# Kernel optimization log

Measured on AMD Instinct MI355X. Metric: run time of the kernel, lower is better.

Reference implementation:

```python
import jax, jax.numpy as jnp
import numpy as np


def setup_inputs() -> dict:
    key = jax.random.key(0)
    ks = jax.random.split(key, 32)
    def rn(i, shape, s=0.02):
        return jax.random.normal(ks[i], shape, dtype=jnp.float32) * s
    z = lambda n: jnp.zeros((n,), dtype=jnp.float32)
    return {
        'c2': rn(0, (8, 256, 112, 112), 1.0),
        'c3': rn(1, (8, 512, 56, 56), 1.0),
        'c4': rn(2, (8, 1024, 28, 28), 1.0),
        'c5': rn(3, (8, 2048, 14, 14), 1.0),
        'lat_w0': rn(4, (256, 256)),  'lat_b0': z(256),
        'lat_w1': rn(5, (512, 256)),  'lat_b1': z(256),
        'lat_w2': rn(6, (1024, 256)), 'lat_b2': z(256),
        'lat_w3': rn(7, (2048, 256)), 'lat_b3': z(256),
        'sp_w1': rn(8, (2048, 512)), 'sp_b1': z(512),
        'sp_w2': rn(9, (512, 4)),    'sp_b2': z(4),
        'qkv_w': rn(10, (256, 768)), 'qkv_b': z(768),
        'proj_w': rn(11, (256, 256)), 'proj_b': z(256),
        'gat_W': rn(12, (4, 256, 256)),
        'gat_a': rn(13, (4, 512)),
        'out_w': rn(14, (1024, 256)), 'out_b': z(256),
        'label_emb': rn(15, (80, 256), 1.0),
        'spec_w1': rn(16, (256, 128)), 'spec_b1': z(128),
        'spec_w2': rn(17, (128, 80)),  'spec_b2': z(80),
        'spat_w1': rn(18, (256, 128)), 'spat_b1': z(128),
        'spat_w2': rn(19, (128, 80)),  'spat_b2': z(80),
        'gate_w': rn(20, (256, 80)), 'gate_b': z(80),
        'unc_w': rn(21, (256, 80)),  'unc_b': z(80),
    }


def _forward(c2, c3, c4, c5,
             lat_w0, lat_b0, lat_w1, lat_b1, lat_w2, lat_b2, lat_w3, lat_b3,
             sp_w1, sp_b1, sp_w2, sp_b2,
             qkv_w, qkv_b, proj_w, proj_b,
             gat_W, gat_a, out_w, out_b, label_emb,
             spec_w1, spec_b1, spec_w2, spec_b2,
             spat_w1, spat_b1, spat_w2, spat_b2,
             gate_w, gate_b, unc_w, unc_b):
    B = c2.shape[0]
    L = label_emb.shape[0]
    C = 256
    # --- DynamicScaleAwareFPN ---
    pooled = c5.mean(axis=(2, 3))                                   # [B,2048]
    sw = jax.nn.softmax(jax.nn.relu(pooled @ sp_w1 + sp_b1) @ sp_w2 + sp_b2, axis=1)  # [B,4]
    H, W = c2.shape[2], c2.shape[3]
    feats = (c2, c3, c4, c5)
    lws = (lat_w0, lat_w1, lat_w2, lat_w3)
    lbs = (lat_b0, lat_b1, lat_b2, lat_b3)
    fused = jnp.zeros((B, C, H, W), dtype=c2.dtype)
    for i in range(4):  # fixed 4 scales
        l = jnp.einsum('bchw,cd->bdhw', feats[i], lws[i]) + lbs[i][None, :, None, None]
        if l.shape[2] != H or l.shape[3] != W:
            l = jax.image.resize(l, (B, C, H, W), method='bilinear')  # align_corners=False
        fused = fused + l * sw[:, i, None, None, None]
    # --- DeformableAttention (N=H*W > max_tokens=196 -> adaptive pool to 14x14) ---
    th = 14
    x = fused.reshape(B, C, th, H // th, th, W // th).mean(axis=(3, 5))  # exact adaptive avg pool
    x = x.reshape(B, C, th * th).transpose(0, 2, 1)                      # [B,196,C]
    N, nh, hd = th * th, 8, C // 8
    qkv = (x @ qkv_w + qkv_b).reshape(B, N, 3, nh, hd).transpose(2, 0, 3, 1, 4)
    q, k, v = qkv[0], qkv[1], qkv[2]                                     # [B,nh,N,hd]
    attn = jax.nn.softmax(jnp.einsum('bhnd,bhmd->bhnm', q, k) * (hd ** -0.5), axis=-1)
    xo = jnp.einsum('bhnm,bhmd->bhnd', attn, v).transpose(0, 2, 1, 3).reshape(B, N, C)
    xo = xo @ proj_w + proj_b
    gctx = xo.mean(axis=1)                                               # [B,C]
    # --- CrossLabelSemanticGraph (4 GAT heads) ---
    lf = label_emb[None] + gctx[:, None, :]                              # [B,L,C]
    def gat(Wm, avec):
        Wx = lf @ Wm                                                     # [B,L,C]
        # a([Wx_i ; Wx_j]) = Wx_i @ a1 + Wx_j @ a2  (avoids O(L^2*2C) tensor)
        s1 = Wx @ avec[:C]                                               # [B,L]
        s2 = Wx @ avec[C:]                                               # [B,L]
        e = jax.nn.leaky_relu(s1[:, :, None] + s2[:, None, :], 0.2)      # [B,L,L]
        att = jax.nn.softmax(e, axis=2)
        return att @ Wx, att
    heads, atts = jax.vmap(gat)(gat_W, gat_a)                            # [4,B,L,C],[4,B,L,L]
    concat = jnp.moveaxis(heads, 0, 2).reshape(B, L, 4 * C)              # head-order concat
    graph = concat @ out_w + out_b                                       # [B,L,C]
    agg = graph.mean(axis=1)                                             # [B,C]
    # --- SpectralSpatialFusion (dropout inactive at eval) ---
    spec = jax.nn.relu(agg @ spec_w1 + spec_b1) @ spec_w2 + spec_b2
    spat = jax.nn.relu(agg @ spat_w1 + spat_b1) @ spat_w2 + spat_b2
    gate = jax.nn.sigmoid(agg @ gate_w + gate_b)
    logits = gate * spec + (1.0 - gate) * spat
    # --- UncertaintyHead ---
    alpha = jax.nn.softplus(agg @ unc_w + unc_b) + 1.0
    unc = L / jnp.sum(alpha, axis=1, keepdims=True)
    return (logits, spec, spat, gate, unc, sw, atts)


def reference(c2, c3, c4, c5,
              lat_w0, lat_b0, lat_w1, lat_b1, lat_w2, lat_b2, lat_w3, lat_b3,
              sp_w1, sp_b1, sp_w2, sp_b2,
              qkv_w, qkv_b, proj_w, proj_b,
              gat_W, gat_a, out_w, out_b, label_emb,
              spec_w1, spec_b1, spec_w2, spec_b2,
              spat_w1, spat_b1, spat_w2, spat_b2,
              gate_w, gate_b, unc_w, unc_b):
    return _forward(c2, c3, c4, c5,
                    lat_w0, lat_b0, lat_w1, lat_b1, lat_w2, lat_b2, lat_w3, lat_b3,
                    sp_w1, sp_b1, sp_w2, sp_b2,
                    qkv_w, qkv_b, proj_w, proj_b,
                    gat_W, gat_a, out_w, out_b, label_emb,
                    spec_w1, spec_b1, spec_w2, spec_b2,
                    spat_w1, spat_b1, spat_w2, spat_b2,
                    gate_w, gate_b, unc_w, unc_b)
```

## Files before the change

kernel.cpp:

```cpp
#include <hip/hip_runtime.h>
#include <math.h>

typedef __attribute__((ext_vector_type(8))) short bshort8;
typedef __attribute__((ext_vector_type(4))) float f32x4;

#define DI __device__ __forceinline__

DI unsigned short f2bf(float x) {
    unsigned int u = __builtin_bit_cast(unsigned int, x);
    u += 0x7fffu + ((u >> 16) & 1u);
    return (unsigned short)(u >> 16);
}

DI bshort8 pack8(const float* v) {
    bshort8 r;
    #pragma unroll
    for (int j = 0; j < 8; j++) r[j] = (short)f2bf(v[j]);
    return r;
}

DI f32x4 mfma16(bshort8 a, bshort8 b, f32x4 c) {
    return __builtin_amdgcn_mfma_f32_16x16x32_bf16(a, b, c, 0, 0, 0);
}

__device__ const float W14[14][3] = {
    {0.875f, 0.125f, 0.f},
    {0.125f, 0.75f, 0.125f}, {0.125f, 0.75f, 0.125f}, {0.125f, 0.75f, 0.125f},
    {0.125f, 0.75f, 0.125f}, {0.125f, 0.75f, 0.125f}, {0.125f, 0.75f, 0.125f},
    {0.125f, 0.75f, 0.125f}, {0.125f, 0.75f, 0.125f}, {0.125f, 0.75f, 0.125f},
    {0.125f, 0.75f, 0.125f}, {0.125f, 0.75f, 0.125f}, {0.125f, 0.75f, 0.125f},
    {0.125f, 0.875f, 0.f}};
__device__ const float W28[14][4] = {
    {0.5f, 0.4375f, 0.0625f, 0.f},
    {0.0625f, 0.4375f, 0.4375f, 0.0625f}, {0.0625f, 0.4375f, 0.4375f, 0.0625f},
    {0.0625f, 0.4375f, 0.4375f, 0.0625f}, {0.0625f, 0.4375f, 0.4375f, 0.0625f},
    {0.0625f, 0.4375f, 0.4375f, 0.0625f}, {0.0625f, 0.4375f, 0.4375f, 0.0625f},
    {0.0625f, 0.4375f, 0.4375f, 0.0625f}, {0.0625f, 0.4375f, 0.4375f, 0.0625f},
    {0.0625f, 0.4375f, 0.4375f, 0.0625f}, {0.0625f, 0.4375f, 0.4375f, 0.0625f},
    {0.0625f, 0.4375f, 0.4375f, 0.0625f}, {0.0625f, 0.4375f, 0.4375f, 0.0625f},
    {0.0625f, 0.4375f, 0.5f, 0.f}};
__device__ const float W56[14][6] = {
    {0.25f, 0.25f, 0.25f, 0.21875f, 0.03125f, 0.f},
    {0.03125f, 0.21875f, 0.25f, 0.25f, 0.21875f, 0.03125f},
    {0.03125f, 0.21875f, 0.25f, 0.25f, 0.21875f, 0.03125f},
    {0.03125f, 0.21875f, 0.25f, 0.25f, 0.21875f, 0.03125f},
    {0.03125f, 0.21875f, 0.25f, 0.25f, 0.21875f, 0.03125f},
    {0.03125f, 0.21875f, 0.25f, 0.25f, 0.21875f, 0.03125f},
    {0.03125f, 0.21875f, 0.25f, 0.25f, 0.21875f, 0.03125f},
    {0.03125f, 0.21875f, 0.25f, 0.25f, 0.21875f, 0.03125f},
    {0.03125f, 0.21875f, 0.25f, 0.25f, 0.21875f, 0.03125f},
    {0.03125f, 0.21875f, 0.25f, 0.25f, 0.21875f, 0.03125f},
    {0.03125f, 0.21875f, 0.25f, 0.25f, 0.21875f, 0.03125f},
    {0.03125f, 0.21875f, 0.25f, 0.25f, 0.21875f, 0.03125f},
    {0.03125f, 0.21875f, 0.25f, 0.25f, 0.21875f, 0.03125f},
    {0.03125f, 0.21875f, 0.25f, 0.25f, 0.25f, 0.f}};

template <int N, int C, int TAPS>
__global__ __launch_bounds__(256) void pool_elem(
    const float* __restrict__ src, float* __restrict__ dst)
{
    unsigned id = blockIdx.x * 256u + threadIdx.x;
    unsigned p = id / 196u;
    unsigned r = id - p * 196u;
    unsigned ti = r / 14u, tj = r - ti * 14u;
    unsigned b = p / C, cin = p - b * C;
    const float* plane = src + (size_t)p * (N * N);
    float acc = 0.f;
    if constexpr (N == 112) {
        const float4* p4 = (const float4*)(plane + (size_t)(ti * 8) * 112 + tj * 8);
        #pragma unroll
        for (int i = 0; i < 8; i++) {
            float4 u = p4[i * 28];
            float4 v = p4[i * 28 + 1];
            acc += (u.x + u.y) + (u.z + u.w) + (v.x + v.y) + (v.z + v.w);
        }
        acc *= (1.f / 64.f);
    } else {
        constexpr int STRIDE = N / 14;
        const float (*WT)[TAPS] = (N == 14) ? (const float (*)[TAPS])W14
                                : (N == 28) ? (const float (*)[TAPS])W28
                                            : (const float (*)[TAPS])W56;
        int hs = (int)(STRIDE * ti) - 1; if (hs < 0) hs = 0;
        int ws = (int)(STRIDE * tj) - 1; if (ws < 0) ws = 0;
        float wh[TAPS], ww[TAPS];
        #pragma unroll
        for (int i = 0; i < TAPS; i++) { wh[i] = WT[ti][i]; ww[i] = WT[tj][i]; }
        #pragma unroll
        for (int i = 0; i < TAPS; i++) {
            int hi = hs + i; if (hi > N - 1) hi = N - 1;
            const float* row = plane + (size_t)hi * N;
            float rs = 0.f;
            #pragma unroll
            for (int j = 0; j < TAPS; j++) {
                int wj = ws + j; if (wj > N - 1) wj = N - 1;
                rs += ww[j] * row[wj];
            }
            acc += wh[i] * rs;
        }
    }
    dst[(size_t)cin * 1568 + b * 196 + r] = acc;
}

__global__ __launch_bounds__(256) void c5_mean(
    const float* __restrict__ c5, float* __restrict__ pooled)
{
    int wid = threadIdx.x >> 6, lane = threadIdx.x & 63;
    int p = blockIdx.x * 4 + wid;
    const float* plane = c5 + (size_t)p * 196;
    float v = plane[lane] + plane[64 + lane] + plane[128 + lane];
    if (lane < 4) v += plane[192 + lane];
    #pragma unroll
    for (int off = 32; off > 0; off >>= 1) v += __shfl_xor(v, off, 64);
    if (lane == 0) pooled[p] = v * (1.f / 196.f);
}

__global__ __launch_bounds__(512) void sw_part(
    const float* __restrict__ pooled, const float* __restrict__ sp_w1,
    float* __restrict__ partial)
{
    int b = blockIdx.x, kc = blockIdx.y, t = threadIdx.x;
    __shared__ float ps[256];
    if (t < 256) ps[t] = pooled[b * 2048 + kc * 256 + t];
    __syncthreads();
    float acc = 0.f;
    const float* w = sp_w1 + (size_t)(kc * 256) * 512 + t;
    #pragma unroll 4
    for (int c = 0; c < 256; c++) acc += ps[c] * w[(size_t)c * 512];
    partial[((size_t)b * 8 + kc) * 512 + t] = acc;
}

__global__ __launch_bounds__(512) void sw_fin(
    const float* __restrict__ partial, const float* __restrict__ sp_b1,
    const float* __restrict__ sp_w2, const float* __restrict__ sp_b2,
    const float* __restrict__ lb0, const float* __restrict__ lb1,
    const float* __restrict__ lb2, const float* __restrict__ lb3,
    float* __restrict__ sw_out, float* __restrict__ beff)
{
    int b = blockIdx.x, t = threadIdx.x;
    __shared__ float h[512];
    __shared__ float s4s[4];
    __shared__ float swl[4];
    float a = sp_b1[t];
    #pragma unroll
    for (int kc = 0; kc < 8; kc++) a += partial[((size_t)b * 8 + kc) * 512 + t];
    h[t] = fmaxf(a, 0.f);
    __syncthreads();
    int wv = t >> 6, lane = t & 63;
    if (wv < 4) {
        float acc = 0.f;
        #pragma unroll
        for (int i = 0; i < 8; i++) {
            int idx = lane + 64 * i;
            acc += h[idx] * sp_w2[idx * 4 + wv];
        }
        #pragma unroll
        for (int off = 32; off > 0; off >>= 1) acc += __shfl_xor(acc, off, 64);
        if (lane == 0) s4s[wv] = acc + sp_b2[wv];
    }
    __syncthreads();
    if (t == 0) {
        float mx = fmaxf(fmaxf(s4s[0], s4s[1]), fmaxf(s4s[2], s4s[3]));
        float e0 = expf(s4s[0] - mx), e1 = expf(s4s[1] - mx);
        float e2 = expf(s4s[2] - mx), e3 = expf(s4s[3] - mx);
        float inv = 1.f / (e0 + e1 + e2 + e3);
        swl[0] = e0 * inv; swl[1] = e1 * inv; swl[2] = e2 * inv; swl[3] = e3 * inv;
        for (int o = 0; o < 4; o++) sw_out[b * 4 + o] = swl[o];
    }
    __syncthreads();
    if (t < 256)
        beff[b * 256 + t] = swl[0] * lb0[t] + swl[1] * lb1[t] + swl[2] * lb2[t] + swl[3] * lb3[t];
}

__global__ __launch_bounds__(256) void xtok_init(
    const float* __restrict__ beff, float* __restrict__ xtok)
{
    int m = blockIdx.x, c = threadIdx.x;
    xtok[(size_t)m * 256 + c] = beff[(m / 196) * 256 + c];
}

__global__ __launch_bounds__(256) void lateral_slice(
    const float* __restrict__ pf0, const float* __restrict__ pf1,
    const float* __restrict__ pf2, const float* __restrict__ pf3,
    const float* __restrict__ w0, const float* __restrict__ w1,
    const float* __restrict__ w2, const float* __restrict__ w3,
    const float* __restrict__ sw, float* __restrict__ xtok)
{
    const int sArr[8]    = {0, 1, 2, 2, 3, 3, 3, 3};
    const int koffArr[8] = {0, 0, 0, 512, 0, 512, 1024, 1536};
    const int klenArr[8] = {256, 512, 512, 512, 512, 512, 512, 512};
    int sl = blockIdx.y;
    int s = sArr[sl], koff = koffArr[sl], klen = klenArr[sl];
    const float* pf = (s == 0) ? pf0 : (s == 1) ? pf1 : (s == 2) ? pf2 : pf3;
    const float* W  = (s == 0) ? w0  : (s == 1) ? w1  : (s == 2) ? w2  : w3;

    int mt = blockIdx.x % 49, nt = blockIdx.x / 49;
    int m0 = mt * 32, n0 = nt * 64;
    __shared__ alignas(16) unsigned short As[1024];
    __shared__ alignas(16) unsigned short Bs[2048];
    int t = threadIdx.x, lane = t & 63, wid = t >> 6;
    int wm = wid >> 1, wn = wid & 1;
    f32x4 acc0 = {0, 0, 0, 0}, acc1 = {0, 0, 0, 0};

    int f = t & 63;
    int mA = m0 + ((t >> 6) & 1) * 16 + (f & 15);
    int kbA = (f >> 4) * 8;
    int nB = n0 + (t >> 6) * 16 + (f & 15);
    int kbB = (f >> 4) * 8;
    float swv = sw[(mA / 196) * 4 + s];

    float ar[8], br[8];
    auto loadA = [&](int k0) {
        if (t < 128) {
            const float* base = pf + (size_t)(koff + k0 + kbA) * 1568 + mA;
            #pragma unroll
            for (int j = 0; j < 8; j++) ar[j] = base[(size_t)j * 1568] * swv;
        }
    };
    auto loadB = [&](int k0) {
        const float* base = W + (size_t)(koff + k0 + kbB) * 256 + nB;
        #pragma unroll
        for (int j = 0; j < 8; j++) br[j] = base[(size_t)j * 256];
    };

    loadA(0); loadB(0);
    for (int k0 = 0; k0 < klen; k0 += 32) {
        if (t < 128) *(bshort8*)&As[(((t >> 6) & 1) * 512 + f * 8)] = pack8(ar);
        *(bshort8*)&Bs[((t >> 6) * 512 + f * 8)] = pack8(br);
        __syncthreads();
        if (k0 + 32 < klen) { loadA(k0 + 32); loadB(k0 + 32); }
        bshort8 av = *(const bshort8*)&As[wm * 512 + lane * 8];
        bshort8 bv0 = *(const bshort8*)&Bs[(wn * 2 + 0) * 512 + lane * 8];
        bshort8 bv1 = *(const bshort8*)&Bs[(wn * 2 + 1) * 512 + lane * 8];
        acc0 = mfma16(av, bv0, acc0);
        acc1 = mfma16(av, bv1, acc1);
        __syncthreads();
    }
    int col0 = n0 + wn * 32 + (lane & 15);
    int rbase = m0 + wm * 16 + ((lane >> 4) << 2);
    #pragma unroll
    for (int r = 0; r < 4; r++) {
        int m = rbase + r;
        atomicAdd(&xtok[(size_t)m * 256 + col0], acc0[r]);
        atomicAdd(&xtok[(size_t)m * 256 + col0 + 16], acc1[r]);
    }
}

template <bool B_IS_KXN>
__global__ __launch_bounds__(256) void gemm_kernel(
    const float* __restrict__ Ab, int lda, long long sAy, long long sAz,
    const float* __restrict__ Bb, int ldb, long long sBy, long long sBz,
    float* __restrict__ Cb, int ldc, long long sCy, long long sCz,
    const float* __restrict__ bias, int M, int N, int K,
    float alpha, int mtiles)
{
    const float* A = Ab + blockIdx.y * sAy + blockIdx.z * sAz;
    const float* B = Bb + blockIdx.y * sBy + blockIdx.z * sBz;
    float* C = Cb + blockIdx.y * sCy + blockIdx.z * sCz;
    int mt = blockIdx.x % mtiles, nt = blockIdx.x / mtiles;
    int m0 = mt * 32, n0 = nt * 64;
    __shared__ alignas(16) unsigned short As[1024];
    __shared__ alignas(16) unsigned short Bs[2048];
    int t = threadIdx.x, lane = t & 63, wid = t >> 6;
    int wm = wid >> 1, wn = wid & 1;
    f32x4 acc0 = {0, 0, 0, 0}, acc1 = {0, 0, 0, 0};

    int f = t & 63;
    int mA = m0 + ((t >> 6) & 1) * 16 + (f & 15);
    int kbA = (f >> 4) * 8;
    int nB = n0 + (t >> 6) * 16 + (f & 15);
    int kbB = (f >> 4) * 8;

    float ar[8], br[8];
    auto loadA = [&](int k0) {
        if (t < 128) {
            int kb = k0 + kbA;
            if (mA < M && kb + 8 <= K) {
                const float4* p = (const float4*)(A + (size_t)mA * lda + kb);
                float4 u = p[0], v = p[1];
                ar[0] = u.x; ar[1] = u.y; ar[2] = u.z; ar[3] = u.w;
                ar[4] = v.x; ar[5] = v.y; ar[6] = v.z; ar[7] = v.w;
            } else {
                #pragma unroll
                for (int j = 0; j < 8; j++) {
                    int k = kb + j;
                    ar[j] = (mA < M && k < K) ? A[(size_t)mA * lda + k] : 0.f;
                }
            }
        }
    };
    auto loadB = [&](int k0) {
        int kb = k0 + kbB;
        if constexpr (B_IS_KXN) {
            #pragma unroll
            for (int j = 0; j < 8; j++) {
                int k = kb + j;
                br[j] = (k < K && nB < N) ? B[(size_t)k * ldb + nB] : 0.f;
            }
        } else {
            if (nB < N && kb + 8 <= K) {
                const float4* p = (const float4*)(B + (size_t)nB * ldb + kb);
                float4 u = p[0], v = p[1];
                br[0] = u.x; br[1] = u.y; br[2] = u.z; br[3] = u.w;
                br[4] = v.x; br[5] = v.y; br[6] = v.z; br[7] = v.w;
            } else {
                #pragma unroll
                for (int j = 0; j < 8; j++) {
                    int k = kb + j;
                    br[j] = (nB < N && k < K) ? B[(size_t)nB * ldb + k] : 0.f;
                }
            }
        }
    };

    loadA(0); loadB(0);
    for (int k0 = 0; k0 < K; k0 += 32) {
        if (t < 128) *(bshort8*)&As[(((t >> 6) & 1) * 512 + f * 8)] = pack8(ar);
        *(bshort8*)&Bs[((t >> 6) * 512 + f * 8)] = pack8(br);
        __syncthreads();
        if (k0 + 32 < K) { loadA(k0 + 32); loadB(k0 + 32); }
        bshort8 av = *(const bshort8*)&As[wm * 512 + lane * 8];
        bshort8 bv0 = *(const bshort8*)&Bs[(wn * 2 + 0) * 512 + lane * 8];
        bshort8 bv1 = *(const bshort8*)&Bs[(wn * 2 + 1) * 512 + lane * 8];
        acc0 = mfma16(av, bv0, acc0);
        acc1 = mfma16(av, bv1, acc1);
        __syncthreads();
    }
    int col0 = n0 + wn * 32 + (lane & 15);
    int rbase = m0 + wm * 16 + ((lane >> 4) << 2);
    #pragma unroll
    for (int r = 0; r < 4; r++) {
        int m = rbase + r;
        if (m < M) {
            if (col0 < N) {
                float v = acc0[r] * alpha;
                if (bias) v += bias[col0];
                C[(size_t)m * ldc + col0] = v;
            }
            int c1 = col0 + 16;
            if (c1 < N) {
                float v = acc1[r] * alpha;
                if (bias) v += bias[c1];
                C[(size_t)m * ldc + c1] = v;
            }
        }
    }
}

__global__ __launch_bounds__(256) void attn_softmax(float* __restrict__ S)
{
    int wid = threadIdx.x >> 6, lane = threadIdx.x & 63;
    size_t row = (size_t)blockIdx.x * 4 + wid;
    float* p = S + row * 196;
    float v0 = p[lane];
    float v1 = p[64 + lane];
    float v2 = p[128 + lane];
    float v3 = (lane < 4) ? p[192 + lane] : -1e30f;
    float mx = fmaxf(fmaxf(v0, v1), fmaxf(v2, v3));
    #pragma unroll
    for (int off = 32; off > 0; off >>= 1) mx = fmaxf(mx, __shfl_xor(mx, off, 64));
    float e0 = expf(v0 - mx), e1 = expf(v1 - mx), e2 = expf(v2 - mx);
    float e3 = (lane < 4) ? expf(v3 - mx) : 0.f;
    float sum = e0 + e1 + e2 + e3;
    #pragma unroll
    for (int off = 32; off > 0; off >>= 1) sum += __shfl_xor(sum, off, 64);
    float inv = 1.f / sum;
    p[lane] = e0 * inv;
    p[64 + lane] = e1 * inv;
    p[128 + lane] = e2 * inv;
    if (lane < 4) p[192 + lane] = e3 * inv;
}

__global__ __launch_bounds__(256) void xo_part(
    const float* __restrict__ xo, float* __restrict__ xopart)
{
    int b = blockIdx.x, g = blockIdx.y, t = threadIdx.x;
    const float* base = xo + ((size_t)b * 196 + g * 28) * 256 + t;
    float s = 0.f;
    #pragma unroll
    for (int n = 0; n < 28; n++) s += base[(size_t)n * 256];
    xopart[(b * 7 + g) * 256 + t] = s;
}

__global__ __launch_bounds__(256) void gctx_part(
    const float* __restrict__ xopart, const float* __restrict__ proj_w,
    float* __restrict__ gpart)
{
    int b = blockIdx.x, kc = blockIdx.y, t = threadIdx.x;
    __shared__ float xm[64];
    if (t < 64) {
        float s = 0.f;
        #pragma unroll
        for (int g = 0; g < 7; g++) s += xopart[(b * 7 + g) * 256 + kc * 64 + t];
        xm[t] = s * (1.f / 196.f);
    }
    __syncthreads();
    float acc = 0.f;
    const float* w = proj_w + (size_t)(kc * 64) * 256 + t;
    #pragma unroll 8
    for (int j = 0; j < 64; j++) acc += xm[j] * w[(size_t)j * 256];
    gpart[(b * 4 + kc) * 256 + t] = acc;
}

__global__ __launch_bounds__(256) void lf_write(
    const float* __restrict__ gpart, const float* __restrict__ proj_b,
    const float* __restrict__ lemb, float* __restrict__ lf)
{
    int b = blockIdx.x, l = blockIdx.y, t = threadIdx.x;
    float g = proj_b[t] + gpart[(b * 4 + 0) * 256 + t] + gpart[(b * 4 + 1) * 256 + t]
            + gpart[(b * 4 + 2) * 256 + t] + gpart[(b * 4 + 3) * 256 + t];
    lf[((size_t)b * 80 + l) * 256 + t] = lemb[l * 256 + t] + g;
}

__global__ __launch_bounds__(256) void wa2(
    const float* __restrict__ gat_W, const float* __restrict__ gat_a,
    float* __restrict__ Wa)
{
    int h = blockIdx.x, q = blockIdx.y;
    int t = threadIdx.x, w = t >> 6, lane = t & 63;
    __shared__ float a1[256], a2[256];
    a1[t] = gat_a[h * 512 + t];
    a2[t] = gat_a[h * 512 + 256 + t];
    __syncthreads();
    for (int ci = 0; ci < 16; ci++) {
        int c = q * 64 + w * 16 + ci;
        const float* row = gat_W + (size_t)h * 65536 + (size_t)c * 256;
        float p1 = 0.f, p2 = 0.f;
        #pragma unroll
        for (int jj = 0; jj < 4; jj++) {
            float v = row[lane + 64 * jj];
            p1 += v * a1[lane + 64 * jj];
            p2 += v * a2[lane + 64 * jj];
        }
        #pragma unroll
        for (int off = 32; off > 0; off >>= 1) {
            p1 += __shfl_xor(p1, off, 64);
            p2 += __shfl_xor(p2, off, 64);
        }
        if (lane == 0) { Wa[h * 512 + c] = p1; Wa[h * 512 + 256 + c] = p2; }
    }
}

__global__ __launch_bounds__(256) void s12_kernel(
    const float* __restrict__ lf, const float* __restrict__ Wa,
    float* __restrict__ s12)
{
    int l = blockIdx.x, b = blockIdx.y, t = threadIdx.x, w = t >> 6, lane = t & 63;
    __shared__ float row[256];
    row[t] = lf[((size_t)b * 80 + l) * 256 + t];
    __syncthreads();
    #pragma unroll
    for (int pp = 0; pp < 2; pp++) {
        int pair = w * 2 + pp;
        float p = 0.f;
        #pragma unroll
        for (int jj = 0; jj < 4; jj++) {
            int c = lane + 64 * jj;
            p += row[c] * Wa[pair * 256 + c];
        }
        #pragma unroll
        for (int off = 32; off > 0; off >>= 1) p += __shfl_xor(p, off, 64);
        if (lane == 0) s12[(b * 8 + pair) * 80 + l] = p;
    }
}

__global__ __launch_bounds__(256) void gat_rows(
    const float* __restrict__ s12, float* __restrict__ atts)
{
    int b = blockIdx.x, h = blockIdx.y, z = blockIdx.z;
    int t = threadIdx.x, w = t >> 6, lane = t & 63;
    int i = z * 4 + w;
    float s1i = s12[(b * 8 + h * 2) * 80 + i];
    const float* s2 = s12 + (b * 8 + h * 2 + 1) * 80;
    float v0 = s1i + s2[lane]; v0 = v0 > 0.f ? v0 : 0.2f * v0;
    float v1 = -1e30f;
    if (lane < 16) { v1 = s1i + s2[64 + lane]; v1 = v1 > 0.f ? v1 : 0.2f * v1; }
    float mx = fmaxf(v0, v1);
    #pragma unroll
    for (int off = 32; off > 0; off >>= 1) mx = fmaxf(mx, __shfl_xor(mx, off, 64));
    float e0 = expf(v0 - mx), e1 = (lane < 16) ? expf(v1 - mx) : 0.f;
    float sum = e0 + e1;
    #pragma unroll
    for (int off = 32; off > 0; off >>= 1) sum += __shfl_xor(sum, off, 64);
    float inv = 1.f / sum;
    float* orow = atts + (size_t)h * 51200 + b * 6400 + i * 80;
    orow[lane] = e0 * inv;
    if (lane < 16) orow[64 + lane] = e1 * inv;
}

__global__ __launch_bounds__(256) void amlf_kernel(
    const float* __restrict__ atts, const float* __restrict__ lf,
    float* __restrict__ amlf)
{
    int b = blockIdx.x, h = blockIdx.y, t = threadIdx.x;
    __shared__ float am[80];
    if (t < 80) {
        const float* base = atts + (size_t)h * 51200 + b * 6400 + t;
        float acc = 0.f;
        for (int l = 0; l < 80; l++) acc += base[l * 80];
        am[t] = acc * (1.f / 80.f);
    }
    __syncthreads();
    float acc = 0.f;
    const float* lfb = lf + (size_t)b * 80 * 256 + t;
    #pragma unroll 4
    for (int l = 0; l < 80; l++) acc += am[l] * lfb[(size_t)l * 256];
    amlf[(b * 4 + h) * 256 + t] = acc;
}

__global__ __launch_bounds__(256) void hm_part(
    const float* __restrict__ amlf, const float* __restrict__ gat_W,
    float* __restrict__ hmpart)
{
    int b = blockIdx.x, h = blockIdx.y, kc = blockIdx.z, t = threadIdx.x;
    __shared__ float av[64];
    if (t < 64) av[t] = amlf[(b * 4 + h) * 256 + kc * 64 + t];
    __syncthreads();
    float acc = 0.f;
    const float* w = gat_W + (size_t)h * 65536 + (size_t)(kc * 64) * 256 + t;
    #pragma unroll 8
    for (int j = 0; j < 64; j++) acc += av[j] * w[(size_t)j * 256];
    hmpart[((b * 4 + h) * 4 + kc) * 256 + t] = acc;
}

__global__ __launch_bounds__(256) void as_part(
    const float* __restrict__ hmpart, const float* __restrict__ out_w,
    float* __restrict__ aspart)
{
    int b = blockIdx.x, kc = blockIdx.y, t = threadIdx.x;
    __shared__ float hv[64];
    if (t < 64) {
        int hk = kc * 64 + t;
        int h = hk >> 8, c = hk & 255;
        const float* p = hmpart + ((size_t)(b * 4 + h) * 4) * 256 + c;
        hv[t] = p[0] + p[256] + p[512] + p[768];
    }
    __syncthreads();
    float acc = 0.f;
    const float* w = out_w + (size_t)(kc * 64) * 256 + t;
    #pragma unroll 8
    for (int j = 0; j < 64; j++) acc += hv[j] * w[(size_t)j * 256];
    aspart[(b * 16 + kc) * 256 + t] = acc;
}

__global__ __launch_bounds__(256) void final2(
    const float* __restrict__ aspart, const float* __restrict__ out_b,
    const float* __restrict__ spec_w1, const float* __restrict__ spec_b1,
    const float* __restrict__ spec_w2, const float* __restrict__ spec_b2,
    const float* __restrict__ spat_w1, const float* __restrict__ spat_b1,
    const float* __restrict__ spat_w2, const float* __restrict__ spat_b2,
    const float* __restrict__ gate_w, const float* __restrict__ gate_b,
    const float* __restrict__ unc_w, const float* __restrict__ unc_b,
    float* __restrict__ out)
{
    int b = blockIdx.x, t = threadIdx.x;
    __shared__ float a_s[256], h1[128], h2[128];
    __shared__ float spv[80], stv[80], gzv[80], alph[80];
    float acc = out_b[t];
    #pragma unroll
    for (int kc = 0; kc < 16; kc++) acc += aspart[(b * 16 + kc) * 256 + t];
    a_s[t] = acc;
    __syncthreads();
    {
        int o = t & 127;
        const float* w1 = (t < 128) ? spec_w1 : spat_w1;
        float a1 = (t < 128) ? spec_b1[o] : spat_b1[o];
        #pragma unroll 4
        for (int c = 0; c < 256; c++) a1 += a_s[c] * w1[c * 128 + o];
        if (t < 128) h1[o] = fmaxf(a1, 0.f); else h2[o] = fmaxf(a1, 0.f);
    }
    __syncthreads();
    if (t < 80) {
        float sp = spec_b2[t];
        for (int c = 0; c < 128; c++) sp += h1[c] * spec_w2[c * 80 + t];
        float gz = gate_b[t];
        #pragma unroll 4
        for (int c = 0; c < 256; c++) gz += a_s[c] * gate_w[c * 80 + t];
        spv[t] = sp; gzv[t] = gz;
    } else if (t >= 128 && t < 208) {
        int o = t - 128;
        float st = spat_b2[o];
        for (int c = 0; c < 128; c++) st += h2[c] * spat_w2[c * 80 + o];
        float uz = unc_b[o];
        #pragma unroll 4
        for (int c = 0; c < 256; c++) uz += a_s[c] * unc_w[c * 80 + o];
        stv[o] = st; alph[o] = log1pf(expf(uz)) + 1.f;
    }
    __syncthreads();
    if (t < 80) {
        float g = 1.f / (1.f + expf(-gzv[t]));
        out[b * 80 + t] = g * spv[t] + (1.f - g) * stv[t];
        out[640 + b * 80 + t] = spv[t];
        out[1280 + b * 80 + t] = stv[t];
        out[1920 + b * 80 + t] = g;
    }
    __syncthreads();
    if (t == 0) {
        float s = 0.f;
        for (int l = 0; l < 80; l++) s += alph[l];
        out[2560 + b] = 80.f / s;
    }
}

extern "C" void kernel_launch(void* const* d_in, const int* in_sizes, int n_in,
                              void* d_out, int out_size, void* d_ws, size_t ws_size,
                              hipStream_t stream)
{
    (void)in_sizes; (void)n_in; (void)out_size; (void)ws_size;
    const float* c2 = (const float*)d_in[0];
    const float* c3 = (const float*)d_in[1];
    const float* c4 = (const float*)d_in[2];
    const float* c5 = (const float*)d_in[3];
    const float* lat_w0 = (const float*)d_in[4];
    const float* lat_b0 = (const float*)d_in[5];
    const float* lat_w1 = (const float*)d_in[6];
    const float* lat_b1 = (const float*)d_in[7];
    const float* lat_w2 = (const float*)d_in[8];
    const float* lat_b2 = (const float*)d_in[9];
    const float* lat_w3 = (const float*)d_in[10];
    const float* lat_b3 = (const float*)d_in[11];
    const float* sp_w1 = (const float*)d_in[12];
    const float* sp_b1 = (const float*)d_in[13];
    const float* sp_w2 = (const float*)d_in[14];
    const float* sp_b2 = (const float*)d_in[15];
    const float* qkv_w = (const float*)d_in[16];
    const float* qkv_b = (const float*)d_in[17];
    const float* proj_w = (const float*)d_in[18];
    const float* proj_b = (const float*)d_in[19];
    const float* gat_W = (const float*)d_in[20];
    const float* gat_a = (const float*)d_in[21];
    const float* out_w = (const float*)d_in[22];
    const float* out_b = (const float*)d_in[23];
    const float* label_emb = (const float*)d_in[24];
    const float* spec_w1 = (const float*)d_in[25];
    const float* spec_b1 = (const float*)d_in[26];
    const float* spec_w2 = (const float*)d_in[27];
    const float* spec_b2 = (const float*)d_in[28];
    const float* spat_w1 = (const float*)d_in[29];
    const float* spat_b1 = (const float*)d_in[30];
    const float* spat_w2 = (const float*)d_in[31];
    const float* spat_b2 = (const float*)d_in[32];
    const float* gate_w = (const float*)d_in[33];
    const float* gate_b = (const float*)d_in[34];
    const float* unc_w = (const float*)d_in[35];
    const float* unc_b = (const float*)d_in[36];

    float* out = (float*)d_out;
    float* ws = (float*)d_ws;

    float* pf0    = ws + 0;
    float* pf1    = ws + 401408;
    float* pf2    = ws + 1204224;
    float* pf3    = ws + 2809856;
    float* pooled = ws + 6021120;
    float* beff   = ws + 6037504;
    float* swpart = ws + 6039552;
    float* qkv    = ws + 0;
    float* S      = ws + 1204224;
    float* xo     = ws + 3662848;
    float* lf     = ws + 4064256;
    float* Wa     = ws + 4228096;
    float* xopart = ws + 4230144;
    float* gpart  = ws + 4244480;
    float* s12    = ws + 4252672;
    float* amlf   = ws + 4257792;
    float* hmpart = ws + 4265984;
    float* aspart = ws + 4298752;
    float* xtok   = ws + 6106112;

    float* swp  = out + 2568;
    float* atts = out + 2600;

    pool_elem<112, 256, 8><<<1568, 256, 0, stream>>>(c2, pf0);
    pool_elem<56, 512, 6><<<3136, 256, 0, stream>>>(c3, pf1);
    pool_elem<28, 1024, 4><<<6272, 256, 0, stream>>>(c4, pf2);
    pool_elem<14, 2048, 3><<<12544, 256, 0, stream>>>(c5, pf3);
    c5_mean<<<4096, 256, 0, stream>>>(c5, pooled);
    sw_part<<<dim3(8, 8), 512, 0, stream>>>(pooled, sp_w1, swpart);
    sw_fin<<<8, 512, 0, stream>>>(swpart, sp_b1, sp_w2, sp_b2,
                                  lat_b0, lat_b1, lat_b2, lat_b3, swp, beff);
    xtok_init<<<1568, 256, 0, stream>>>(beff, xtok);
    lateral_slice<<<dim3(196, 8), 256, 0, stream>>>(pf0, pf1, pf2, pf3,
                                                    lat_w0, lat_w1, lat_w2, lat_w3,
                                                    swp, xtok);
    gemm_kernel<true><<<dim3(49 * 12, 1, 1), 256, 0, stream>>>(
        xtok, 256, 0, 0, qkv_w, 768, 0, 0, qkv, 768, 0, 0,
        qkv_b, 1568, 768, 256, 1.f, 49);
    gemm_kernel<false><<<dim3(7 * 4, 8, 8), 256, 0, stream>>>(
        qkv, 768, 150528, 32, qkv + 256, 768, 150528, 32,
        S, 196, 307328, 38416, nullptr, 196, 196, 32, 0.17677669529663687f, 7);
    attn_softmax<<<3136, 256, 0, stream>>>(S);
    gemm_kernel<true><<<dim3(7, 8, 8), 256, 0, stream>>>(
        S, 196, 307328, 38416, qkv + 512, 768, 150528, 32,
        xo, 256, 50176, 32, nullptr, 196, 32, 196, 1.f, 7);
    xo_part<<<dim3(8, 7), 256, 0, stream>>>(xo, xopart);
    gctx_part<<<dim3(8, 4), 256, 0, stream>>>(xopart, proj_w, gpart);
    lf_write<<<dim3(8, 80), 256, 0, stream>>>(gpart, proj_b, label_emb, lf);
    wa2<<<dim3(4, 4), 256, 0, stream>>>(gat_W, gat_a, Wa);
    s12_kernel<<<dim3(80, 8), 256, 0, stream>>>(lf, Wa, s12);
    gat_rows<<<dim3(8, 4, 20), 256, 0, stream>>>(s12, atts);
    amlf_kernel<<<dim3(8, 4), 256, 0, stream>>>(atts, lf, amlf);
    hm_part<<<dim3(8, 4, 4), 256, 0, stream>>>(amlf, gat_W, hmpart);
    as_part<<<dim3(8, 16), 256, 0, stream>>>(hmpart, out_w, aspart);
    final2<<<8, 256, 0, stream>>>(aspart, out_b,
        spec_w1, spec_b1, spec_w2, spec_b2,
        spat_w1, spat_b1, spat_w2, spat_b2,
        gate_w, gate_b, unc_w, unc_b, out);
}
```

Before: 540.2 us.

## Fuse lf_write into s12 and split final head into parallel kernels

Merges the label-feature write into the s12 score kernel, removing one launch and a global round trip of lf. The serial 8-block final2 kernel is split into as_fin, mlp1, mlp2 and final_comb, which spread the small head GEMVs over more blocks with split-K reductions. A few loop unroll factors are also raised. The split adds three extra launches on the tail in exchange for more parallelism in each step.

```diff
diff --git a/kernel.cpp b/kernel.cpp
--- a/kernel.cpp
+++ b/kernel.cpp
@@ -124,7 +124,7 @@
     __syncthreads();
     float acc = 0.f;
     const float* w = sp_w1 + (size_t)(kc * 256) * 512 + t;
-    #pragma unroll 4
+    #pragma unroll 8
     for (int c = 0; c < 256; c++) acc += ps[c] * w[(size_t)c * 512];
     partial[((size_t)b * 8 + kc) * 512 + t] = acc;
 }
@@ -401,16 +401,6 @@
     gpart[(b * 4 + kc) * 256 + t] = acc;
 }
 
-__global__ __launch_bounds__(256) void lf_write(
-    const float* __restrict__ gpart, const float* __restrict__ proj_b,
-    const float* __restrict__ lemb, float* __restrict__ lf)
-{
-    int b = blockIdx.x, l = blockIdx.y, t = threadIdx.x;
-    float g = proj_b[t] + gpart[(b * 4 + 0) * 256 + t] + gpart[(b * 4 + 1) * 256 + t]
-            + gpart[(b * 4 + 2) * 256 + t] + gpart[(b * 4 + 3) * 256 + t];
-    lf[((size_t)b * 80 + l) * 256 + t] = lemb[l * 256 + t] + g;
-}
-
 __global__ __launch_bounds__(256) void wa2(
     const float* __restrict__ gat_W, const float* __restrict__ gat_a,
     float* __restrict__ Wa)
@@ -440,13 +430,19 @@
     }
 }
 
-__global__ __launch_bounds__(256) void s12_kernel(
-    const float* __restrict__ lf, const float* __restrict__ Wa,
-    float* __restrict__ s12)
-{
-    int l = blockIdx.x, b = blockIdx.y, t = threadIdx.x, w = t >> 6, lane = t & 63;
+__global__ __launch_bounds__(256) void lf_s12(
+    const float* __restrict__ gpart, const float* __restrict__ proj_b,
+    const float* __restrict__ lemb, const float* __restrict__ Wa,
+    float* __restrict__ lf, float* __restrict__ s12)
+{
+    int l = blockIdx.x, b = blockIdx.y, t = threadIdx.x;
+    int w = t >> 6, lane = t & 63;
     __shared__ float row[256];
-    row[t] = lf[((size_t)b * 80 + l) * 256 + t];
+    float g = proj_b[t] + gpart[(b * 4 + 0) * 256 + t] + gpart[(b * 4 + 1) * 256 + t]
+            + gpart[(b * 4 + 2) * 256 + t] + gpart[(b * 4 + 3) * 256 + t];
+    float v = lemb[l * 256 + t] + g;
+    lf[((size_t)b * 80 + l) * 256 + t] = v;
+    row[t] = v;
     __syncthreads();
     #pragma unroll
     for (int pp = 0; pp < 2; pp++) {
@@ -496,13 +492,14 @@
     if (t < 80) {
         const float* base = atts + (size_t)h * 51200 + b * 6400 + t;
         float acc = 0.f;
+        #pragma unroll 8
         for (int l = 0; l < 80; l++) acc += base[l * 80];
         am[t] = acc * (1.f / 80.f);
     }
     __syncthreads();
     float acc = 0.f;
     const float* lfb = lf + (size_t)b * 80 * 256 + t;
-    #pragma unroll 4
+    #pragma unroll 8
     for (int l = 0; l < 80; l++) acc += am[l] * lfb[(size_t)l * 256];
     amlf[(b * 4 + h) * 256 + t] = acc;
 }
@@ -542,56 +539,93 @@
     aspart[(b * 16 + kc) * 256 + t] = acc;
 }
 
-__global__ __launch_bounds__(256) void final2(
+__global__ __launch_bounds__(256) void as_fin(
     const float* __restrict__ aspart, const float* __restrict__ out_b,
+    float* __restrict__ a_s)
+{
+    int b = blockIdx.x, t = threadIdx.x;
+    float acc = out_b[t];
+    #pragma unroll
+    for (int kc = 0; kc < 16; kc++) acc += aspart[(b * 16 + kc) * 256 + t];
+    a_s[b * 256 + t] = acc;
+}
+
+__global__ __launch_bounds__(256) void mlp1(
+    const float* __restrict__ a_s,
     const float* __restrict__ spec_w1, const float* __restrict__ spec_b1,
+    const float* __restrict__ spat_w1, const float* __restrict__ spat_b1,
+    float* __restrict__ hbuf)
+{
+    int b = blockIdx.x, which = blockIdx.y, t = threadIdx.x;
+    const float* w1 = which ? spat_w1 : spec_w1;
+    const float* b1 = which ? spat_b1 : spec_b1;
+    __shared__ float as_s[256];
+    __shared__ float red[256];
+    as_s[t] = a_s[b * 256 + t];
+    __syncthreads();
+    int o = t & 63, ks = t >> 6;
+    #pragma unroll
+    for (int p = 0; p < 2; p++) {
+        int oo = p * 64 + o;
+        float acc = 0.f;
+        const float* w = w1 + (size_t)(ks * 64) * 128 + oo;
+        #pragma unroll 8
+        for (int j = 0; j < 64; j++) acc += as_s[ks * 64 + j] * w[(size_t)j * 128];
+        red[t] = acc;
+        __syncthreads();
+        if (ks == 0) {
+            float v = red[o] + red[64 + o] + red[128 + o] + red[192 + o] + b1[oo];
+            hbuf[(b * 2 + which) * 128 + oo] = fmaxf(v, 0.f);
+        }
+        __syncthreads();
+    }
+}
+
+__global__ __launch_bounds__(256) void mlp2(
+    const float* __restrict__ a_s, const float* __restrict__ hbuf,
     const float* __restrict__ spec_w2, const float* __restrict__ spec_b2,
-    const float* __restrict__ spat_w1, const float* __restrict__ spat_b1,
     const float* __restrict__ spat_w2, const float* __restrict__ spat_b2,
     const float* __restrict__ gate_w, const float* __restrict__ gate_b,
     const float* __restrict__ unc_w, const float* __restrict__ unc_b,
-    float* __restrict__ out)
+    float* __restrict__ fv)
+{
+    int b = blockIdx.x, head = blockIdx.y, t = threadIdx.x;
+    __shared__ float src[256];
+    __shared__ float red[240];
+    const float* w; const float* bias; int K;
+    if (head == 0)      { w = spec_w2; bias = spec_b2; K = 128; }
+    else if (head == 1) { w = spat_w2; bias = spat_b2; K = 128; }
+    else if (head == 2) { w = gate_w; bias = gate_b; K = 256; }
+    else                { w = unc_w;  bias = unc_b;  K = 256; }
+    if (head < 2) { if (t < 128) src[t] = hbuf[(b * 2 + head) * 128 + t]; }
+    else src[t] = a_s[b * 256 + t];
+    __syncthreads();
+    if (t < 240) {
+        int o = t % 80, s = t / 80;
+        int k0 = (K * s) / 3, k1 = (K * (s + 1)) / 3;
+        float acc = 0.f;
+        #pragma unroll 8
+        for (int k = k0; k < k1; k++) acc += src[k] * w[(size_t)k * 80 + o];
+        red[t] = acc;
+    }
+    __syncthreads();
+    if (t < 80) fv[(b * 4 + head) * 80 + t] = red[t] + red[80 + t] + red[160 + t] + bias[t];
+}
+
+__global__ __launch_bounds__(128) void final_comb(
+    const float* __restrict__ fv, float* __restrict__ out)
 {
     int b = blockIdx.x, t = threadIdx.x;
-    __shared__ float a_s[256], h1[128], h2[128];
-    __shared__ float spv[80], stv[80], gzv[80], alph[80];
-    float acc = out_b[t];
-    #pragma unroll
-    for (int kc = 0; kc < 16; kc++) acc += aspart[(b * 16 + kc) * 256 + t];
-    a_s[t] = acc;
-    __syncthreads();
-    {
-        int o = t & 127;
-        const float* w1 = (t < 128) ? spec_w1 : spat_w1;
-        float a1 = (t < 128) ? spec_b1[o] : spat_b1[o];
-        #pragma unroll 4
-        for (int c = 0; c < 256; c++) a1 += a_s[c] * w1[c * 128 + o];
-        if (t < 128) h1[o] = fmaxf(a1, 0.f); else h2[o] = fmaxf(a1, 0.f);
-    }
-    __syncthreads();
+    __shared__ float alph[80];
     if (t < 80) {
-        float sp = spec_b2[t];
-        for (int c = 0; c < 128; c++) sp += h1[c] * spec_w2[c * 80 + t];
-        float gz = gate_b[t];
-        #pragma unroll 4
-        for (int c = 0; c < 256; c++) gz += a_s[c] * gate_w[c * 80 + t];
-        spv[t] = sp; gzv[t] = gz;
-    } else if (t >= 128 && t < 208) {
-        int o = t - 128;
-        float st = spat_b2[o];
-        for (int c = 0; c < 128; c++) st += h2[c] * spat_w2[c * 80 + o];
-        float uz = unc_b[o];
-        #pragma unroll 4
-        for (int c = 0; c < 256; c++) uz += a_s[c] * unc_w[c * 80 + o];
-        stv[o] = st; alph[o] = log1pf(expf(uz)) + 1.f;
-    }
-    __syncthreads();
-    if (t < 80) {
-        float g = 1.f / (1.f + expf(-gzv[t]));
-        out[b * 80 + t] = g * spv[t] + (1.f - g) * stv[t];
-        out[640 + b * 80 + t] = spv[t];
-        out[1280 + b * 80 + t] = stv[t];
+        float sp = fv[(b * 4 + 0) * 80 + t], st = fv[(b * 4 + 1) * 80 + t];
+        float gz = fv[(b * 4 + 2) * 80 + t], uz = fv[(b * 4 + 3) * 80 + t];
+        float g = 1.f / (1.f + expf(-gz));
+        out[b * 80 + t] = g * sp + (1.f - g) * st;
+        out[640 + b * 80 + t] = sp;
+        out[1280 + b * 80 + t] = st;
         out[1920 + b * 80 + t] = g;
+        alph[t] = log1pf(expf(uz)) + 1.f;
     }
     __syncthreads();
     if (t == 0) {
@@ -665,6 +699,9 @@
     float* amlf   = ws + 4257792;
     float* hmpart = ws + 4265984;
     float* aspart = ws + 4298752;
+    float* a_sb   = ws + 4331520;
+    float* hbuf   = ws + 4333568;
+    float* fv     = ws + 4335616;
     float* xtok   = ws + 6106112;
 
     float* swp  = out + 2568;
@@ -694,15 +731,16 @@
         xo, 256, 50176, 32, nullptr, 196, 32, 196, 1.f, 7);
     xo_part<<<dim3(8, 7), 256, 0, stream>>>(xo, xopart);
     gctx_part<<<dim3(8, 4), 256, 0, stream>>>(xopart, proj_w, gpart);
-    lf_write<<<dim3(8, 80), 256, 0, stream>>>(gpart, proj_b, label_emb, lf);
     wa2<<<dim3(4, 4), 256, 0, stream>>>(gat_W, gat_a, Wa);
-    s12_kernel<<<dim3(80, 8), 256, 0, stream>>>(lf, Wa, s12);
+    lf_s12<<<dim3(80, 8), 256, 0, stream>>>(gpart, proj_b, label_emb, Wa, lf, s12);
     gat_rows<<<dim3(8, 4, 20), 256, 0, stream>>>(s12, atts);
     amlf_kernel<<<dim3(8, 4), 256, 0, stream>>>(atts, lf, amlf);
     hm_part<<<dim3(8, 4, 4), 256, 0, stream>>>(amlf, gat_W, hmpart);
     as_part<<<dim3(8, 16), 256, 0, stream>>>(hmpart, out_w, aspart);
-    final2<<<8, 256, 0, stream>>>(aspart, out_b,
-        spec_w1, spec_b1, spec_w2, spec_b2,
-        spat_w1, spat_b1, spat_w2, spat_b2,
-        gate_w, gate_b, unc_w, unc_b, out);
-}
+    as_fin<<<8, 256, 0, stream>>>(aspart, out_b, a_sb);
+    mlp1<<<dim3(8, 2), 256, 0, stream>>>(a_sb, spec_w1, spec_b1, spat_w1, spat_b1, hbuf);
+    mlp2<<<dim3(8, 4), 256, 0, stream>>>(a_sb, hbuf,
+        spec_w2, spec_b2, spat_w2, spat_b2,
+        gate_w, gate_b, unc_w, unc_b, fv);
+    final_comb<<<8, 128, 0, stream>>>(fv, out);
+}
```

Result: faster. 485.3 us (-10.2%).
